# Optimization experiments

Hardware: AMD Instinct MI355X
Metric: run time of the kernel (lower is better)

## Reference

```python
import jax, jax.numpy as jnp
import numpy as np

B, S, D_IN, D_OUT = 4, 4096, 2048, 2048
DELTA_A = 0.0
DELTA_W = 0.05


def setup_inputs() -> dict:
    key = jax.random.key(0)
    kx, kw = jax.random.split(key)
    # xavier_uniform bound for [out, in] weight
    bound = float(np.sqrt(6.0 / (D_IN + D_OUT)))
    x = jax.random.normal(kx, (B, S, D_IN), dtype=jnp.float32)
    W = jax.random.uniform(kw, (D_OUT, D_IN), dtype=jnp.float32, minval=-bound, maxval=bound)
    b = jnp.zeros((D_OUT,), dtype=jnp.float32)
    return {"x": x, "W": W, "b": b}


def reference(x, W, b):
    # --- activation ternarization (BitNet STE); pre_ln=False -> identity ---
    ax = jnp.abs(x)
    thr_a = DELTA_A * jnp.mean(ax, axis=-1, keepdims=True)
    xa = jnp.where(ax < thr_a, jnp.zeros_like(x), jnp.sign(x))
    x_final = x + jax.lax.stop_gradient(xa - x)

    # --- weight ternarization with per-row alpha scale ---
    Wc = W - jnp.mean(W, axis=1, keepdims=True)
    aWc = jnp.abs(Wc)
    thr_w = DELTA_W * jnp.mean(aWc, axis=1, keepdims=True)
    code = jnp.where(aWc < thr_w, jnp.zeros_like(Wc), jnp.sign(Wc))
    nz = (code != 0).astype(Wc.dtype)
    alpha = jnp.sum(aWc * nz, axis=1, keepdims=True) / jnp.clip(
        jnp.sum(nz, axis=1, keepdims=True), 1.0, None
    )
    Wq = alpha * code
    W_final = W + jax.lax.stop_gradient(Wq - W)

    # F.linear: y = x @ W^T + b
    return jnp.einsum("bsd,od->bso", x_final, W_final) + b
```

## Files before the change

kernel.cpp:

```cpp
#include <hip/hip_runtime.h>
#include <stdint.h>

#define K_DIM   2048
#define N_DIM   2048
#define M_DIM   16384
#define DELTA_W 0.05f

#define BM 128
#define BN 256
#define BK 64
#define NT (K_DIM / BK)

typedef __attribute__((ext_vector_type(4))) int i32x4;

__device__ __forceinline__ void async_copy16(const void* g, void* l) {
    __builtin_amdgcn_global_load_lds(
        (__attribute__((address_space(1))) void*)g,
        (__attribute__((address_space(3))) void*)l,
        16, 0, 0);
}

__device__ __forceinline__ float block_sum_256(float v, float* sm) {
#pragma unroll
    for (int o = 32; o > 0; o >>= 1) v += __shfl_down(v, o, 64);
    const int lane = threadIdx.x & 63;
    const int w    = threadIdx.x >> 6;
    __syncthreads();
    if (lane == 0) sm[w] = v;
    __syncthreads();
    return sm[0] + sm[1] + sm[2] + sm[3];
}

__global__ __launch_bounds__(256) void quant_kernel(
    const float* __restrict__ W, const float* __restrict__ x,
    int8_t* __restrict__ code, float* __restrict__ alpha,
    int8_t* __restrict__ xq)
{
    __shared__ float sm[4];
    const int t = threadIdx.x;

    if (blockIdx.x < N_DIM) {
        const int row = blockIdx.x;
        const float* Wr = W + (size_t)row * K_DIM;

        float v[8];
        float s = 0.f;
#pragma unroll
        for (int i = 0; i < 8; ++i) { v[i] = Wr[t + i * 256]; s += v[i]; }
        const float mean = block_sum_256(s, sm) * (1.0f / K_DIM);

        float sa = 0.f;
#pragma unroll
        for (int i = 0; i < 8; ++i) sa += fabsf(v[i] - mean);
        const float thr = DELTA_W * (block_sum_256(sa, sm) * (1.0f / K_DIM));

        float ssum = 0.f, scnt = 0.f;
        int8_t q[8];
#pragma unroll
        for (int i = 0; i < 8; ++i) {
            const float c = v[i] - mean;
            const float a = fabsf(c);
            int8_t qv = 0;
            if (a >= thr) qv = (int8_t)((c > 0.f) - (c < 0.f));
            q[i] = qv;
            if (qv != 0) { ssum += a; scnt += 1.0f; }
        }
        const float num = block_sum_256(ssum, sm);
        const float den = block_sum_256(scnt, sm);
        if (t == 0) alpha[row] = num / fmaxf(den, 1.0f);

#pragma unroll
        for (int i = 0; i < 8; ++i)
            code[(size_t)row * K_DIM + t + i * 256] = q[i];
    } else {
        const int blk = blockIdx.x - N_DIM;
        const int base = blk * 1024 + t;
        const float4* xin = (const float4*)x;
        char4* xo = (char4*)xq;
#pragma unroll
        for (int i = 0; i < 4; ++i) {
            const float4 f = xin[base + i * 256];
            char4 c;
            c.x = (char)((f.x > 0.f) - (f.x < 0.f));
            c.y = (char)((f.y > 0.f) - (f.y < 0.f));
            c.z = (char)((f.z > 0.f) - (f.z < 0.f));
            c.w = (char)((f.w > 0.f) - (f.w < 0.f));
            xo[base + i * 256] = c;
        }
    }
}

__global__ __launch_bounds__(512, 4) void gemm_kernel(
    const int8_t* __restrict__ A, const int8_t* __restrict__ Bt,
    const float* __restrict__ alpha, const float* __restrict__ bias,
    float* __restrict__ out)
{
    __shared__ __align__(16) int8_t As[2][BM * BK];
    __shared__ __align__(16) int8_t Bs[2][BN * BK];

    const int tid  = threadIdx.x;
    const int lane = tid & 63;
    const int wv   = tid >> 6;
    const int wm   = (wv >> 2) * 64;
    const int wn   = (wv & 3) * 64;
    const int fr   = lane & 15;
    const int q    = lane >> 4;
    const int cs16 = (q ^ ((fr >> 1) & 3)) * 16;

    const int bid = blockIdx.x;
    const int xcd = bid & 7;
    const int idx = bid >> 3;
    const int tileN = (idx & 7) * BN;
    const int tileM = ((idx >> 3) + (xcd << 4)) * BM;

    const int ra = tid >> 2;
    const int ca = (tid & 3) ^ ((ra >> 1) & 3);
    const unsigned a_off = (unsigned)(tileM + ra) * K_DIM + ca * 16;
    unsigned b_off[2];
#pragma unroll
    for (int e = 0; e < 2; ++e) {
        const int s  = e * 512 + tid;
        const int rb = s >> 2;
        const int cb = (s & 3) ^ ((rb >> 1) & 3);
        b_off[e] = (unsigned)(tileN + rb) * K_DIM + cb * 16;
    }

    i32x4 acc[4][4] = {};
    i32x4 af[4], bf[4];

#define STAGE(nbp, kk0) do {                                                   \
    async_copy16(A  + a_off    + (kk0), &As[nbp][tid * 16]);                   \
    async_copy16(Bt + b_off[0] + (kk0), &Bs[nbp][tid * 16]);                   \
    async_copy16(Bt + b_off[1] + (kk0), &Bs[nbp][8192 + tid * 16]);            \
} while (0)

    STAGE(0, 0);

    int k1 = 0;

#define GROUP(bp, DS, WV) {                                                    \
    const int8_t* Ac = As[(bp)];                                               \
    const int8_t* Bc = Bs[(bp)];                                               \
    if (DS) { STAGE((bp) ^ 1, k1); }                                           \
    asm volatile("s_waitcnt vmcnt(" WV ")\n\ts_barrier" ::: "memory");         \
    _Pragma("unroll")                                                          \
    for (int i = 0; i < 4; ++i)                                                \
        af[i] = *(const i32x4*)(Ac + (wm + i * 16 + fr) * 64 + cs16);          \
    _Pragma("unroll")                                                          \
    for (int j = 0; j < 4; ++j)                                                \
        bf[j] = *(const i32x4*)(Bc + (wn + j * 16 + fr) * 64 + cs16);          \
    _Pragma("unroll")                                                          \
    for (int i = 0; i < 4; ++i) {                                              \
        _Pragma("unroll")                                                      \
        for (int j = 0; j < 4; ++j)                                            \
            acc[i][j] = __builtin_amdgcn_mfma_i32_16x16x64_i8(                 \
                af[i], bf[j], acc[i][j], 0, 0, 0);                             \
    }                                                                          \
    asm volatile("s_barrier" ::: "memory");                                    \
}

#pragma unroll 1
    for (int t = 0; t < NT - 1; ++t) {
        k1 = (t + 1) * BK;
        GROUP(t & 1, 1, "3");
    }
    GROUP((NT - 1) & 1, 0, "0");

#undef GROUP
#undef STAGE

    const int cl = lane & 15;
    const int qr = lane >> 4;
#pragma unroll
    for (int j = 0; j < 4; ++j) {
        const int n  = tileN + wn + j * 16 + cl;
        const float al = alpha[n];
        const float bi = bias[n];
#pragma unroll
        for (int i = 0; i < 4; ++i) {
            const int mbase = tileM + wm + i * 16 + qr * 4;
#pragma unroll
            for (int r = 0; r < 4; ++r) {
                out[(size_t)(mbase + r) * N_DIM + n] =
                    al * (float)acc[i][j][r] + bi;
            }
        }
    }
}

extern "C" void kernel_launch(void* const* d_in, const int* in_sizes, int n_in,
                              void* d_out, int out_size, void* d_ws, size_t ws_size,
                              hipStream_t stream) {
    const float* x = (const float*)d_in[0];
    const float* W = (const float*)d_in[1];
    const float* b = (const float*)d_in[2];
    float* out = (float*)d_out;

    int8_t* xq    = (int8_t*)d_ws;
    int8_t* wcode = xq + (size_t)M_DIM * K_DIM;
    float*  alpha = (float*)(wcode + (size_t)N_DIM * K_DIM);

    quant_kernel<<<N_DIM + 8192, 256, 0, stream>>>(W, x, wcode, alpha, xq);

    gemm_kernel<<<1024, dim3(512), 0, stream>>>(xq, wcode, alpha, b, out);
}
```

Measured before the change: 307.2 us.

## Triple-buffer GEMM LDS tiles and software-pipeline fragment reads with MFMAs

Moves the int8 GEMM main loop from double to triple buffering in LDS, so global-to-LDS copies run two K-tiles ahead. LDS fragment reads for the next tile are interleaved between halves of the current tile's MFMAs using double-buffered register fragments, and the trailing barrier per iteration is dropped. Launch bounds are lowered to 2 blocks per SM to allow the extra registers, which reduces occupancy and raises LDS use per block.

```diff
diff --git a/kernel.cpp b/kernel.cpp
--- a/kernel.cpp
+++ b/kernel.cpp
@@ -90,13 +90,13 @@
     }
 }
 
-__global__ __launch_bounds__(512, 4) void gemm_kernel(
+__global__ __launch_bounds__(512, 2) void gemm_kernel(
     const int8_t* __restrict__ A, const int8_t* __restrict__ Bt,
     const float* __restrict__ alpha, const float* __restrict__ bias,
     float* __restrict__ out)
 {
-    __shared__ __align__(16) int8_t As[2][BM * BK];
-    __shared__ __align__(16) int8_t Bs[2][BN * BK];
+    __shared__ __align__(16) int8_t As[3][BM * BK];
+    __shared__ __align__(16) int8_t Bs[3][BN * BK];
 
     const int tid  = threadIdx.x;
     const int lane = tid & 63;
@@ -126,47 +126,63 @@
     }
 
     i32x4 acc[4][4] = {};
-    i32x4 af[4], bf[4];
-
-#define STAGE(nbp, kk0) do {                                                   \
-    async_copy16(A  + a_off    + (kk0), &As[nbp][tid * 16]);                   \
-    async_copy16(Bt + b_off[0] + (kk0), &Bs[nbp][tid * 16]);                   \
-    async_copy16(Bt + b_off[1] + (kk0), &Bs[nbp][8192 + tid * 16]);            \
+    i32x4 af[2][4], bf[2][4];
+
+#define STAGE(BC, kk0) do {                                                    \
+    async_copy16(A  + a_off    + (kk0), &As[BC][tid * 16]);                    \
+    async_copy16(Bt + b_off[0] + (kk0), &Bs[BC][tid * 16]);                    \
+    async_copy16(Bt + b_off[1] + (kk0), &Bs[BC][8192 + tid * 16]);             \
 } while (0)
 
-    STAGE(0, 0);
-
-    int k1 = 0;
-
-#define GROUP(bp, DS, WV) {                                                    \
-    const int8_t* Ac = As[(bp)];                                               \
-    const int8_t* Bc = Bs[(bp)];                                               \
-    if (DS) { STAGE((bp) ^ 1, k1); }                                           \
-    asm volatile("s_waitcnt vmcnt(" WV ")\n\ts_barrier" ::: "memory");         \
+#define RD(P, BC) {                                                            \
     _Pragma("unroll")                                                          \
     for (int i = 0; i < 4; ++i)                                                \
-        af[i] = *(const i32x4*)(Ac + (wm + i * 16 + fr) * 64 + cs16);          \
+        af[P][i] = *(const i32x4*)(&As[BC][(wm + i * 16 + fr) * 64] + cs16);   \
     _Pragma("unroll")                                                          \
     for (int j = 0; j < 4; ++j)                                                \
-        bf[j] = *(const i32x4*)(Bc + (wn + j * 16 + fr) * 64 + cs16);          \
+        bf[P][j] = *(const i32x4*)(&Bs[BC][(wn + j * 16 + fr) * 64] + cs16);   \
+}
+
+#define SUBMM(P, I0) {                                                         \
     _Pragma("unroll")                                                          \
-    for (int i = 0; i < 4; ++i) {                                              \
+    for (int i = I0; i < I0 + 2; ++i) {                                        \
         _Pragma("unroll")                                                      \
         for (int j = 0; j < 4; ++j)                                            \
             acc[i][j] = __builtin_amdgcn_mfma_i32_16x16x64_i8(                 \
-                af[i], bf[j], acc[i][j], 0, 0, 0);                             \
+                af[P][i], bf[P][j], acc[i][j], 0, 0, 0);                       \
     }                                                                          \
-    asm volatile("s_barrier" ::: "memory");                                    \
-}
+}
+
+#define GROUP(T, P, BNX, BS, DS, WV) {                                         \
+    if (DS) { STAGE(BS, (T + 2) * BK); }                                       \
+    SUBMM(P, 0);                                                               \
+    asm volatile("s_waitcnt vmcnt(" WV ")\n\ts_barrier" ::: "memory");         \
+    RD(P ^ 1, BNX);                                                            \
+    SUBMM(P, 2);                                                               \
+}
+
+    STAGE(0, 0);
+    STAGE(1, BK);
+    asm volatile("s_waitcnt vmcnt(3)\n\ts_barrier" ::: "memory");
+    RD(0, 0);
 
 #pragma unroll 1
-    for (int t = 0; t < NT - 1; ++t) {
-        k1 = (t + 1) * BK;
-        GROUP(t & 1, 1, "3");
-    }
-    GROUP((NT - 1) & 1, 0, "0");
+    for (int u = 0; u < 5; ++u) {
+        const int t6 = u * 6;
+        GROUP(t6 + 0, 0, 1, 2, 1, "3");
+        GROUP(t6 + 1, 1, 2, 0, 1, "3");
+        GROUP(t6 + 2, 0, 0, 1, 1, "3");
+        GROUP(t6 + 3, 1, 1, 2, 1, "3");
+        GROUP(t6 + 4, 0, 2, 0, 1, "3");
+        GROUP(t6 + 5, 1, 0, 1, 1, "3");
+    }
+    GROUP(30, 0, 1, 0, 0, "0");
+    SUBMM(1, 0);
+    SUBMM(1, 2);
 
 #undef GROUP
+#undef SUBMM
+#undef RD
 #undef STAGE
 
     const int cl = lane & 15;
```

Result: slower. 325.1 us (+5.8%).
